# Kernel optimization log

Measured on AMD Instinct MI355X. Metric: run time of the kernel, lower is better.

Reference implementation:

```python
import math
import jax, jax.numpy as jnp
import numpy as np

N_HEAD = 16

def setup_inputs() -> dict:
    key = jax.random.key(0)
    ks = jax.random.split(key, 7)
    B, T, C = 4, 2048, 1024
    QL, KVL = 256, 256
    s = 0.02
    return {
        "x":     jax.random.normal(ks[0], (B, T, C), jnp.float32),
        "W_dq":  jax.random.normal(ks[1], (QL, C), jnp.float32) * s,
        "W_uq":  jax.random.normal(ks[2], (C, QL), jnp.float32) * s,
        "W_dkv": jax.random.normal(ks[3], (KVL, C), jnp.float32) * s,
        "W_uk":  jax.random.normal(ks[4], (C, KVL), jnp.float32) * s,
        "W_uv":  jax.random.normal(ks[5], (C, KVL), jnp.float32) * s,
        "W_o":   jax.random.normal(ks[6], (C, C), jnp.float32) * s,
    }

def reference(x, W_dq, W_uq, W_dkv, W_uk, W_uv, W_o):
    B, T, C = x.shape
    nh = N_HEAD
    hs = C // nh
    kvl = W_dkv.shape[0]
    # Absorbed projection matrices (training path: recomputed each call)
    # k_eff: (nh, hs, kvl); v_eff: (nh, kvl, hs)
    k_eff = (W_dq.T @ W_uq.T @ W_uk).reshape(nh, hs, kvl)
    v_eff = (W_uv.T @ W_o.T).reshape(kvl, nh, hs).transpose(1, 0, 2)
    # Latent KV cache: (B, T, kvl)
    c_kv = x @ W_dkv.T
    # Queries: (B, nh, T, hs)
    q = (x @ W_dq.T @ W_uq.T).reshape(B, T, nh, hs).transpose(0, 2, 1, 3)
    # Scores: q @ k_eff @ c_kv^T / sqrt(hs) -> (B, nh, T, T)
    q_lat = jnp.einsum('bhtd,hdl->bhtl', q, k_eff)
    attn = jnp.einsum('bhtl,bsl->bhts', q_lat, c_kv) / math.sqrt(hs)
    causal_mask = jnp.triu(jnp.ones((T, T), bool), k=1)
    attn = jnp.where(causal_mask[None, None], -jnp.inf, attn)
    attn = jax.nn.softmax(attn, axis=-1)  # dropout p=0 -> identity
    # Output: attn @ c_kv @ v_eff -> (B, T, C)
    ctx = jnp.einsum('bhts,bsl->bhtl', attn, c_kv)
    y = jnp.einsum('bhtl,hld->bhtd', ctx, v_eff).transpose(0, 2, 1, 3).reshape(B, T, C)
    return (y, c_kv)
```

## Files before the change

kernel.cpp:

```cpp
#include <hip/hip_runtime.h>

typedef unsigned short u16;
typedef __attribute__((ext_vector_type(8))) short short8;
typedef __attribute__((ext_vector_type(4))) float f32x4;

#define MFMA_BF16 __builtin_amdgcn_mfma_f32_16x16x32_bf16

__device__ __forceinline__ u16 f2bf(float f){
  unsigned int u = __builtin_bit_cast(unsigned int, f);
  u += 0x7fffu + ((u >> 16) & 1u);
  return (u16)(u >> 16);
}

__device__ __forceinline__ void gld16(const void* g, void* l){
  __builtin_amdgcn_global_load_lds(
      (const __attribute__((address_space(1))) unsigned int*)g,
      (__attribute__((address_space(3))) unsigned int*)l, 16, 0, 0);
}

__global__ void k_transpose4(const float* __restrict__ s0, float* __restrict__ d0,
                             const float* __restrict__ s1, float* __restrict__ d1,
                             const float* __restrict__ s2, float* __restrict__ d2,
                             const float* __restrict__ s3, float* __restrict__ d3)
{
  __shared__ float tile[32][33];
  int z = blockIdx.z;
  const float* src = z == 0 ? s0 : z == 1 ? s1 : z == 2 ? s2 : s3;
  float* dst       = z == 0 ? d0 : z == 1 ? d1 : z == 2 ? d2 : d3;
  int rows = z == 0 ? 256 : 1024, cols = z == 0 ? 1024 : 256;
  int c0 = blockIdx.x * 32, r0 = blockIdx.y * 32;
  if (c0 >= cols || r0 >= rows) return;
  int tx = threadIdx.x, ty = threadIdx.y;
#pragma unroll
  for (int i = 0; i < 4; ++i){
    int r = ty + i * 8;
    tile[r][tx] = src[(long)(r0 + r) * cols + c0 + tx];
  }
  __syncthreads();
#pragma unroll
  for (int i = 0; i < 4; ++i){
    int r = ty + i * 8;
    dst[(long)(c0 + r) * rows + r0 + tx] = tile[tx][r];
  }
}

__global__ __launch_bounds__(256)
void k_gemm_nt(const float* __restrict__ A, const float* __restrict__ B,
               float* __restrict__ Cf, u16* __restrict__ Cb,
               int M, int N, int K, int lda, int ldb, int ldc,
               long sA, long sB, long sC, float scale)
{
  A += (long)blockIdx.z * sA; B += (long)blockIdx.z * sB;
  if (Cf) Cf += (long)blockIdx.z * sC;
  if (Cb) Cb += (long)blockIdx.z * sC;
  const int n0 = blockIdx.x * 64, m0 = blockIdx.y * 64;
  const int tid = threadIdx.x;
  const int wave = tid >> 6, lane = tid & 63, quad = lane >> 4, l16 = lane & 15;
  __shared__ u16 As[64 * 40];
  __shared__ u16 Bs[64 * 40];
  f32x4 acc[4];
#pragma unroll
  for (int n = 0; n < 4; ++n) acc[n] = (f32x4){0.f, 0.f, 0.f, 0.f};

  const int lr = tid >> 2;
  const int lc = (tid & 3) * 8;
  for (int k0 = 0; k0 < K; k0 += 32){
    {
      const float* pa = &A[(long)(m0 + lr) * lda + k0 + lc];
      float4 a0 = *(const float4*)pa;
      float4 a1 = *(const float4*)(pa + 4);
      short8 pk;
      pk[0]=(short)f2bf(a0.x); pk[1]=(short)f2bf(a0.y); pk[2]=(short)f2bf(a0.z); pk[3]=(short)f2bf(a0.w);
      pk[4]=(short)f2bf(a1.x); pk[5]=(short)f2bf(a1.y); pk[6]=(short)f2bf(a1.z); pk[7]=(short)f2bf(a1.w);
      *(short8*)&As[lr * 40 + lc] = pk;
      const float* pb = &B[(long)(n0 + lr) * ldb + k0 + lc];
      float4 b0 = *(const float4*)pb;
      float4 b1 = *(const float4*)(pb + 4);
      short8 qk;
      qk[0]=(short)f2bf(b0.x); qk[1]=(short)f2bf(b0.y); qk[2]=(short)f2bf(b0.z); qk[3]=(short)f2bf(b0.w);
      qk[4]=(short)f2bf(b1.x); qk[5]=(short)f2bf(b1.y); qk[6]=(short)f2bf(b1.z); qk[7]=(short)f2bf(b1.w);
      *(short8*)&Bs[lr * 40 + lc] = qk;
    }
    __syncthreads();
    short8 a = *(const short8*)&As[(wave * 16 + l16) * 40 + quad * 8];
#pragma unroll
    for (int n = 0; n < 4; ++n){
      short8 b = *(const short8*)&Bs[(n * 16 + l16) * 40 + quad * 8];
      acc[n] = MFMA_BF16(a, b, acc[n], 0, 0, 0);
    }
    __syncthreads();
  }
#pragma unroll
  for (int n = 0; n < 4; ++n)
#pragma unroll
    for (int r = 0; r < 4; ++r){
      int row = m0 + wave * 16 + quad * 4 + r;
      int col = n0 + n * 16 + l16;
      float v = acc[n][r] * scale;
      if (Cf) Cf[(long)row * ldc + col] = v;
      if (Cb) Cb[(long)row * ldc + col] = f2bf(v);
    }
}

__global__ __launch_bounds__(256)
void k_proj(const float* __restrict__ x, const float* __restrict__ Wdq,
            const float* __restrict__ Wdkv, u16* __restrict__ xq,
            float* __restrict__ ckv_f, u16* __restrict__ ckv_bf, u16* __restrict__ ckvT)
{
  const bool is_kv = blockIdx.x >= 4;
  const float* B = is_kv ? Wdkv : Wdq;
  const int n0 = (blockIdx.x & 3) * 64, m0 = blockIdx.y * 64;
  const int tid = threadIdx.x;
  const int wave = tid >> 6, lane = tid & 63, quad = lane >> 4, l16 = lane & 15;
  __shared__ u16 As[64 * 40];
  __shared__ u16 Bs[64 * 40];
  f32x4 acc[4];
#pragma unroll
  for (int n = 0; n < 4; ++n) acc[n] = (f32x4){0.f, 0.f, 0.f, 0.f};

  const int lr = tid >> 2;
  const int lc = (tid & 3) * 8;
  for (int k0 = 0; k0 < 1024; k0 += 32){
    {
      const float* pa = &x[(long)(m0 + lr) * 1024 + k0 + lc];
      float4 a0 = *(const float4*)pa;
      float4 a1 = *(const float4*)(pa + 4);
      short8 pk;
      pk[0]=(short)f2bf(a0.x); pk[1]=(short)f2bf(a0.y); pk[2]=(short)f2bf(a0.z); pk[3]=(short)f2bf(a0.w);
      pk[4]=(short)f2bf(a1.x); pk[5]=(short)f2bf(a1.y); pk[6]=(short)f2bf(a1.z); pk[7]=(short)f2bf(a1.w);
      *(short8*)&As[lr * 40 + lc] = pk;
      const float* pb = &B[(long)(n0 + lr) * 1024 + k0 + lc];
      float4 b0 = *(const float4*)pb;
      float4 b1 = *(const float4*)(pb + 4);
      short8 qk;
      qk[0]=(short)f2bf(b0.x); qk[1]=(short)f2bf(b0.y); qk[2]=(short)f2bf(b0.z); qk[3]=(short)f2bf(b0.w);
      qk[4]=(short)f2bf(b1.x); qk[5]=(short)f2bf(b1.y); qk[6]=(short)f2bf(b1.z); qk[7]=(short)f2bf(b1.w);
      *(short8*)&Bs[lr * 40 + lc] = qk;
    }
    __syncthreads();
    short8 a = *(const short8*)&As[(wave * 16 + l16) * 40 + quad * 8];
#pragma unroll
    for (int n = 0; n < 4; ++n){
      short8 b = *(const short8*)&Bs[(n * 16 + l16) * 40 + quad * 8];
      acc[n] = MFMA_BF16(a, b, acc[n], 0, 0, 0);
    }
    __syncthreads();
  }
  if (!is_kv){
#pragma unroll
    for (int n = 0; n < 4; ++n)
#pragma unroll
      for (int r = 0; r < 4; ++r){
        int row = m0 + wave * 16 + quad * 4 + r;
        int col = n0 + n * 16 + l16;
        xq[(long)row * 256 + col] = f2bf(acc[n][r]);
      }
  } else {
    const int b = (m0 >> 11);
    const int t0 = (m0 & 2047) + wave * 16 + quad * 4;
#pragma unroll
    for (int n = 0; n < 4; ++n){
      int col = n0 + n * 16 + l16;
      u16 pk[4];
#pragma unroll
      for (int r = 0; r < 4; ++r){
        int row = m0 + wave * 16 + quad * 4 + r;
        float v = acc[n][r];
        ckv_f [(long)row * 256 + col] = v;
        ckv_bf[(long)row * 256 + col] = f2bf(v);
        pk[r] = f2bf(v);
      }
      *(uint2*)&ckvT[((long)b * 256 + col) * 2048 + t0] = *(uint2*)pk;
    }
  }
}

__global__ __launch_bounds__(256, 2)
void k_flash(const u16* __restrict__ xq, const u16* __restrict__ Pt,
             const u16* __restrict__ ckv_bf, const u16* __restrict__ ckvT,
             const u16* __restrict__ Vt, float* __restrict__ y)
{
  const int qt = 31 - blockIdx.x, h = blockIdx.y, b = blockIdx.z;
  const int tid = threadIdx.x;
  const int wg = tid >> 6, lane = tid & 63, quad = lane >> 4, l16 = lane & 15;

  __shared__ u16 X0[64 * 256];
  __shared__ u16 X1[256 * 64];

  const int trow = wg * 16 + l16;
  const long tglob = (long)b * 2048 + qt * 64;
  const int sw_t = trow & 7;

  const u16* ckv_b  = ckv_bf + (long)b * 2048 * 256;
  const u16* ckvT_b = ckvT   + (long)b * 256 * 2048;

  const u16* srcA[8]; const u16* srcB[8];
  {
    int l5 = lane >> 5, g32 = lane & 31;
#pragma unroll
    for (int j = 0; j < 8; ++j){
      int s = (wg * 8 + j) * 2 + l5;
      int g = g32 ^ (s & 7);
      srcA[j] = ckv_b + (long)s * 256 + g * 8;
    }
    int l3 = lane >> 3, g8 = lane & 7;
#pragma unroll
    for (int j = 0; j < 8; ++j){
      int l = (wg * 8 + j) * 8 + l3;
      int g = g8 ^ (l & 7);
      srcB[j] = ckvT_b + (long)l * 2048 + g * 8;
    }
  }

  short8 aS[8];
  {
    short8 bq[8];
    const u16* xr = xq + (tglob + trow) * 256;
#pragma unroll
    for (int ks = 0; ks < 8; ++ks)
      bq[ks] = *(const short8*)&xr[ks * 32 + quad * 8];
    const u16* pth = Pt + (long)h * 65536;
#pragma unroll
    for (int mb = 0; mb < 16; ++mb){
      f32x4 acc = (f32x4){0.f, 0.f, 0.f, 0.f};
#pragma unroll
      for (int ks = 0; ks < 8; ++ks){
        short8 pa = *(const short8*)&pth[(mb * 16 + l16) * 256 + ks * 32 + quad * 8];
        acc = MFMA_BF16(pa, bq[ks], acc, 0, 0, 0);
      }
#pragma unroll
      for (int r = 0; r < 4; ++r){
        int l = mb * 16 + quad * 4 + r;
        int cs = (((l >> 3) ^ (l16 & 7)) << 3) | (l & 7);
        X0[trow * 256 + cs] = f2bf(acc[r]);
      }
    }
  }
  __syncthreads();
#pragma unroll
  for (int ks = 0; ks < 8; ++ks){
    int gl = ks * 4 + quad;
    aS[ks] = *(const short8*)&X0[trow * 256 + ((gl ^ sw_t) << 3)];
  }

  float m_t = -1e30f, l_t = 0.f;
  f32x4 oacc[16];
#pragma unroll
  for (int n = 0; n < 16; ++n) oacc[n] = (f32x4){0.f, 0.f, 0.f, 0.f};

  for (int st = 0; st <= qt; ++st){
    __syncthreads();
#pragma unroll
    for (int j = 0; j < 8; ++j)
      gld16(srcA[j] + (long)st * 16384, &X0[(wg * 8 + j) * 512]);
#pragma unroll
    for (int j = 0; j < 8; ++j)
      gld16(srcB[j] + st * 64, &X1[(wg * 8 + j) * 512]);
    __syncthreads();

    f32x4 sacc[4];
#pragma unroll
    for (int mb = 0; mb < 4; ++mb) sacc[mb] = (f32x4){0.f, 0.f, 0.f, 0.f};
#pragma unroll
    for (int ks = 0; ks < 8; ++ks){
#pragma unroll
      for (int mb = 0; mb < 4; ++mb){
        int gl = ks * 4 + quad;
        short8 a = *(const short8*)&X0[(mb * 16 + l16) * 256 + ((gl ^ (l16 & 7)) << 3)];
        sacc[mb] = MFMA_BF16(a, aS[ks], sacc[mb], 0, 0, 0);
      }
    }
    if (st == qt){
      int t = qt * 64 + trow;
#pragma unroll
      for (int mb = 0; mb < 4; ++mb)
#pragma unroll
        for (int r = 0; r < 4; ++r)
          if (st * 64 + mb * 16 + quad * 4 + r > t) sacc[mb][r] = -1e30f;
    }

    float pm[4][4];
    {
      float rm = sacc[0][0];
#pragma unroll
      for (int mb = 0; mb < 4; ++mb)
#pragma unroll
        for (int r = 0; r < 4; ++r) rm = fmaxf(rm, sacc[mb][r]);
      rm = fmaxf(rm, __shfl_xor(rm, 16, 64));
      rm = fmaxf(rm, __shfl_xor(rm, 32, 64));
      float mnew = fmaxf(m_t, rm);
      float alpha = __expf(m_t - mnew);
      m_t = mnew;
      float rs = 0.f;
#pragma unroll
      for (int mb = 0; mb < 4; ++mb)
#pragma unroll
        for (int r = 0; r < 4; ++r){
          float pe = __expf(sacc[mb][r] - mnew);
          pm[mb][r] = pe;
          rs += pe;
        }
      rs += __shfl_xor(rs, 16, 64);
      rs += __shfl_xor(rs, 32, 64);
      l_t = l_t * alpha + rs;
#pragma unroll
      for (int r2 = 0; r2 < 4; ++r2){
        float ar = __shfl(alpha, quad * 4 + r2, 64);
#pragma unroll
        for (int n = 0; n < 16; ++n) oacc[n][r2] *= ar;
      }
    }
    __syncthreads();
#pragma unroll
    for (int mb = 0; mb < 4; ++mb)
#pragma unroll
      for (int r = 0; r < 4; ++r)
        X0[trow * 72 + mb * 16 + quad * 4 + r] = f2bf(pm[mb][r]);
    __syncthreads();

    {
      short8 a0 = *(const short8*)&X0[trow * 72 + quad * 8];
      short8 a1 = *(const short8*)&X0[trow * 72 + 32 + quad * 8];
#pragma unroll
      for (int n = 0; n < 16; ++n){
        int lr_ = n * 16 + l16;
        int swl = lr_ & 7;
        short8 b0 = *(const short8*)&X1[lr_ * 64 + ((quad ^ swl) << 3)];
        short8 b1 = *(const short8*)&X1[lr_ * 64 + (((4 + quad) ^ swl) << 3)];
        oacc[n] = MFMA_BF16(a0, b0, oacc[n], 0, 0, 0);
        oacc[n] = MFMA_BF16(a1, b1, oacc[n], 0, 0, 0);
      }
    }
  }

  __syncthreads();
  {
    float linv = 1.f / l_t;
#pragma unroll
    for (int r = 0; r < 4; ++r){
      float lr_ = __shfl(linv, quad * 4 + r, 64);
#pragma unroll
      for (int n = 0; n < 16; ++n) oacc[n][r] *= lr_;
    }
#pragma unroll
    for (int n = 0; n < 16; ++n)
#pragma unroll
      for (int r = 0; r < 4; ++r){
        int trw = wg * 16 + quad * 4 + r;
        int l = n * 16 + l16;
        int cs = (((l >> 3) ^ (trw & 7)) << 3) | (l & 7);
        X0[trw * 256 + cs] = f2bf(oacc[n][r]);
      }
  }
  __syncthreads();
  {
    const u16* vth = Vt + (long)h * 64 * 256;
    short8 ca[8];
#pragma unroll
    for (int ks = 0; ks < 8; ++ks){
      int gl = ks * 4 + quad;
      ca[ks] = *(const short8*)&X0[trow * 256 + ((gl ^ sw_t) << 3)];
    }
#pragma unroll
    for (int n = 0; n < 4; ++n){
      f32x4 acc = (f32x4){0.f, 0.f, 0.f, 0.f};
#pragma unroll
      for (int ks = 0; ks < 8; ++ks){
        short8 vb = *(const short8*)&vth[(n * 16 + l16) * 256 + ks * 32 + quad * 8];
        acc = MFMA_BF16(ca[ks], vb, acc, 0, 0, 0);
      }
#pragma unroll
      for (int r = 0; r < 4; ++r)
        y[(tglob + wg * 16 + quad * 4 + r) * 1024 + h * 64 + n * 16 + l16] = acc[r];
    }
  }
}

extern "C" void kernel_launch(void* const* d_in, const int* in_sizes, int n_in,
                              void* d_out, int out_size, void* d_ws, size_t ws_size,
                              hipStream_t stream)
{
  (void)in_sizes; (void)n_in; (void)out_size; (void)ws_size;
  const float* x    = (const float*)d_in[0];
  const float* Wdq  = (const float*)d_in[1];
  const float* Wuq  = (const float*)d_in[2];
  const float* Wdkv = (const float*)d_in[3];
  const float* Wuk  = (const float*)d_in[4];
  const float* Wuv  = (const float*)d_in[5];
  const float* Wo   = (const float*)d_in[6];

  float* y_out   = (float*)d_out;
  float* ckv_out = y_out + (size_t)4 * 2048 * 1024;

  char* base = (char*)d_ws;
  float* wdqT   = (float*)(base + 0);
  float* wuqT   = (float*)(base + 1048576);
  float* wukT   = (float*)(base + 2097152);
  float* wuvT   = (float*)(base + 3145728);
  u16*   ckvT   = (u16*)  (base + 0);
  float* t1T    = (float*)(base + 4194304);
  float* keffT  = (float*)(base + 4456448);
  u16*   pt     = (u16*)  (base + 5505024);
  u16*   vt     = (u16*)  (base + 7602176);
  u16*   xq     = (u16*)  (base + 8126464);
  u16*   ckv_bf = (u16*)  (base + 12320768);

  k_transpose4<<<dim3(32, 32, 4), dim3(32, 8), 0, stream>>>(
      Wdq, wdqT, Wuq, wuqT, Wuk, wukT, Wuv, wuvT);

  k_gemm_nt<<<dim3(4, 4, 1), 256, 0, stream>>>(wukT, wuqT, t1T, (u16*)0,
      256, 256, 1024, 1024, 1024, 256, 0, 0, 0, 1.f);
  k_gemm_nt<<<dim3(16, 4, 1), 256, 0, stream>>>(t1T, wdqT, keffT, (u16*)0,
      256, 1024, 256, 256, 256, 1024, 0, 0, 0, 1.f);
  k_gemm_nt<<<dim3(4, 4, 16), 256, 0, stream>>>(keffT, wuqT, (float*)0, pt,
      256, 256, 64, 1024, 1024, 256, 64, 64, 65536, 0.125f);
  k_gemm_nt<<<dim3(4, 16, 1), 256, 0, stream>>>(Wo, wuvT, (float*)0, vt,
      1024, 256, 1024, 1024, 1024, 256, 0, 0, 0, 1.f);

  k_proj<<<dim3(8, 128), 256, 0, stream>>>(x, Wdq, Wdkv, xq, ckv_out, ckv_bf, ckvT);

  k_flash<<<dim3(32, 16, 4), 256, 0, stream>>>(xq, pt, ckv_bf, ckvT, vt, y_out);
}
```

Before: 740.0 us.

## Widen flash attention blocks to 128 query rows with 8 waves sharing KV tiles

The flash kernel now runs 512 threads per block covering 128 query rows, so each latent KV tile loaded into LDS is reused by twice as many waves and total KV traffic roughly halves. Waves skip score and PV work on tiles that lie fully above the causal diagonal. The P tile is written per wave into LDS without the extra block barrier, using packed stores and a swizzle. In exchange the block count halves, register pressure rises under the 512,4 launch bound, and waves near the diagonal sit idle while their block-mates finish the extra tiles.

```diff
diff --git a/kernel.cpp b/kernel.cpp
--- a/kernel.cpp
+++ b/kernel.cpp
@@ -175,12 +175,12 @@
   }
 }
 
-__global__ __launch_bounds__(256, 2)
+__global__ __launch_bounds__(512, 4)
 void k_flash(const u16* __restrict__ xq, const u16* __restrict__ Pt,
              const u16* __restrict__ ckv_bf, const u16* __restrict__ ckvT,
              const u16* __restrict__ Vt, float* __restrict__ y)
 {
-  const int qt = 31 - blockIdx.x, h = blockIdx.y, b = blockIdx.z;
+  const int qt = 15 - (int)blockIdx.x, h = blockIdx.y, b = blockIdx.z;
   const int tid = threadIdx.x;
   const int wg = tid >> 6, lane = tid & 63, quad = lane >> 4, l16 = lane & 15;
 
@@ -188,27 +188,25 @@
   __shared__ u16 X1[256 * 64];
 
   const int trow = wg * 16 + l16;
-  const long tglob = (long)b * 2048 + qt * 64;
-  const int sw_t = trow & 7;
+  const long tglob = (long)b * 2048 + (long)qt * 128;
+  u16* Xq = (wg < 4) ? X0 : X1;
+  const int rloc = trow & 63;
+  const int sw7 = l16 & 7;
 
   const u16* ckv_b  = ckv_bf + (long)b * 2048 * 256;
   const u16* ckvT_b = ckvT   + (long)b * 256 * 2048;
 
-  const u16* srcA[8]; const u16* srcB[8];
+  int offA[4], offB[4];
   {
     int l5 = lane >> 5, g32 = lane & 31;
-#pragma unroll
-    for (int j = 0; j < 8; ++j){
-      int s = (wg * 8 + j) * 2 + l5;
-      int g = g32 ^ (s & 7);
-      srcA[j] = ckv_b + (long)s * 256 + g * 8;
-    }
     int l3 = lane >> 3, g8 = lane & 7;
 #pragma unroll
-    for (int j = 0; j < 8; ++j){
-      int l = (wg * 8 + j) * 8 + l3;
-      int g = g8 ^ (l & 7);
-      srcB[j] = ckvT_b + (long)l * 2048 + g * 8;
+    for (int j = 0; j < 4; ++j){
+      int c = wg * 4 + j;
+      int s = c * 2 + l5;
+      offA[j] = s * 256 + ((g32 ^ (s & 7)) * 8);
+      int l = c * 8 + l3;
+      offB[j] = l * 2048 + ((g8 ^ (l & 7)) * 8);
     }
   }
 
@@ -231,16 +229,15 @@
 #pragma unroll
       for (int r = 0; r < 4; ++r){
         int l = mb * 16 + quad * 4 + r;
-        int cs = (((l >> 3) ^ (l16 & 7)) << 3) | (l & 7);
-        X0[trow * 256 + cs] = f2bf(acc[r]);
-      }
-    }
-  }
-  __syncthreads();
+        int cs = (((l >> 3) ^ sw7) << 3) | (l & 7);
+        Xq[rloc * 256 + cs] = f2bf(acc[r]);
+      }
+    }
+  }
 #pragma unroll
   for (int ks = 0; ks < 8; ++ks){
     int gl = ks * 4 + quad;
-    aS[ks] = *(const short8*)&X0[trow * 256 + ((gl ^ sw_t) << 3)];
+    aS[ks] = *(const short8*)&Xq[rloc * 256 + ((gl ^ sw7) << 3)];
   }
 
   float m_t = -1e30f, l_t = 0.f;
@@ -248,39 +245,41 @@
 #pragma unroll
   for (int n = 0; n < 16; ++n) oacc[n] = (f32x4){0.f, 0.f, 0.f, 0.f};
 
-  for (int st = 0; st <= qt; ++st){
-    __syncthreads();
-#pragma unroll
-    for (int j = 0; j < 8; ++j)
-      gld16(srcA[j] + (long)st * 16384, &X0[(wg * 8 + j) * 512]);
-#pragma unroll
-    for (int j = 0; j < 8; ++j)
-      gld16(srcB[j] + st * 64, &X1[(wg * 8 + j) * 512]);
-    __syncthreads();
-
+  const int nst = 2 * qt + 2;
+  const int tmin_w = qt * 128 + wg * 16;
+
+  for (int st = 0; st < nst; ++st){
+    __syncthreads();
+#pragma unroll
+    for (int j = 0; j < 4; ++j)
+      gld16(ckv_b + (long)st * 16384 + offA[j], &X0[(wg * 4 + j) * 512]);
+#pragma unroll
+    for (int j = 0; j < 4; ++j)
+      gld16(ckvT_b + st * 64 + offB[j], &X1[(wg * 4 + j) * 512]);
+    __syncthreads();
+
+    const bool active = (st * 64 <= tmin_w + 15);
     f32x4 sacc[4];
-#pragma unroll
-    for (int mb = 0; mb < 4; ++mb) sacc[mb] = (f32x4){0.f, 0.f, 0.f, 0.f};
-#pragma unroll
-    for (int ks = 0; ks < 8; ++ks){
-#pragma unroll
-      for (int mb = 0; mb < 4; ++mb){
-        int gl = ks * 4 + quad;
-        short8 a = *(const short8*)&X0[(mb * 16 + l16) * 256 + ((gl ^ (l16 & 7)) << 3)];
-        sacc[mb] = MFMA_BF16(a, aS[ks], sacc[mb], 0, 0, 0);
-      }
-    }
-    if (st == qt){
-      int t = qt * 64 + trow;
-#pragma unroll
-      for (int mb = 0; mb < 4; ++mb)
-#pragma unroll
-        for (int r = 0; r < 4; ++r)
-          if (st * 64 + mb * 16 + quad * 4 + r > t) sacc[mb][r] = -1e30f;
-    }
-
-    float pm[4][4];
-    {
+    if (active){
+#pragma unroll
+      for (int mb = 0; mb < 4; ++mb) sacc[mb] = (f32x4){0.f, 0.f, 0.f, 0.f};
+#pragma unroll
+      for (int ks = 0; ks < 8; ++ks){
+#pragma unroll
+        for (int mb = 0; mb < 4; ++mb){
+          int gl = ks * 4 + quad;
+          short8 a = *(const short8*)&X0[(mb * 16 + l16) * 256 + ((gl ^ (l16 & 7)) << 3)];
+          sacc[mb] = MFMA_BF16(a, aS[ks], sacc[mb], 0, 0, 0);
+        }
+      }
+      if ((st + 1) * 64 > tmin_w + 1){
+        int t = qt * 128 + trow;
+#pragma unroll
+        for (int mb = 0; mb < 4; ++mb)
+#pragma unroll
+          for (int r = 0; r < 4; ++r)
+            if (st * 64 + mb * 16 + quad * 4 + r > t) sacc[mb][r] = -1e30f;
+      }
       float rm = sacc[0][0];
 #pragma unroll
       for (int mb = 0; mb < 4; ++mb)
@@ -297,7 +296,7 @@
 #pragma unroll
         for (int r = 0; r < 4; ++r){
           float pe = __expf(sacc[mb][r] - mnew);
-          pm[mb][r] = pe;
+          sacc[mb][r] = pe;
           rs += pe;
         }
       rs += __shfl_xor(rs, 16, 64);
@@ -311,16 +310,19 @@
       }
     }
     __syncthreads();
-#pragma unroll
-    for (int mb = 0; mb < 4; ++mb)
-#pragma unroll
-      for (int r = 0; r < 4; ++r)
-        X0[trow * 72 + mb * 16 + quad * 4 + r] = f2bf(pm[mb][r]);
-    __syncthreads();
-
-    {
-      short8 a0 = *(const short8*)&X0[trow * 72 + quad * 8];
-      short8 a1 = *(const short8*)&X0[trow * 72 + 32 + quad * 8];
+
+    if (active){
+#pragma unroll
+      for (int mb = 0; mb < 4; ++mb){
+        u16 pk[4];
+#pragma unroll
+        for (int r = 0; r < 4; ++r) pk[r] = f2bf(sacc[mb][r]);
+        int c = mb * 16 + quad * 4;
+        int gr = (c >> 3) ^ sw7;
+        *(uint2*)&X0[trow * 64 + gr * 8 + (c & 7)] = *(uint2*)pk;
+      }
+      short8 a0 = *(const short8*)&X0[trow * 64 + ((quad ^ sw7) << 3)];
+      short8 a1 = *(const short8*)&X0[trow * 64 + (((4 + quad) ^ sw7) << 3)];
 #pragma unroll
       for (int n = 0; n < 16; ++n){
         int lr_ = n * 16 + l16;
@@ -349,17 +351,16 @@
         int trw = wg * 16 + quad * 4 + r;
         int l = n * 16 + l16;
         int cs = (((l >> 3) ^ (trw & 7)) << 3) | (l & 7);
-        X0[trw * 256 + cs] = f2bf(oacc[n][r]);
-      }
-  }
-  __syncthreads();
+        Xq[(trw & 63) * 256 + cs] = f2bf(oacc[n][r]);
+      }
+  }
   {
     const u16* vth = Vt + (long)h * 64 * 256;
     short8 ca[8];
 #pragma unroll
     for (int ks = 0; ks < 8; ++ks){
       int gl = ks * 4 + quad;
-      ca[ks] = *(const short8*)&X0[trow * 256 + ((gl ^ sw_t) << 3)];
+      ca[ks] = *(const short8*)&Xq[rloc * 256 + ((gl ^ sw7) << 3)];
     }
 #pragma unroll
     for (int n = 0; n < 4; ++n){
@@ -419,5 +420,5 @@
 
   k_proj<<<dim3(8, 128), 256, 0, stream>>>(x, Wdq, Wdkv, xq, ckv_out, ckv_bf, ckvT);
 
-  k_flash<<<dim3(32, 16, 4), 256, 0, stream>>>(xq, pt, ckv_bf, ckvT, vt, y_out);
-}
+  k_flash<<<dim3(16, 16, 4), 512, 0, stream>>>(xq, pt, ckv_bf, ckvT, vt, y_out);
+}
```

Result: slower. 885.2 us (+19.6%).

## Load K/V tiles directly from global memory and use per-wave LDS slabs

Applied to the files above, without the earlier changes.

The flash kernel no longer stages the ckv and ckvT tiles into shared memory with global_load_lds and block-wide barriers. Each wave now reads its MFMA operands straight from global memory (relying on L1/L2 for reuse across the four waves) and uses a small private padded LDS slab for its own layout transposes, which removes every __syncthreads. The smaller shared-memory footprint lets the launch bounds ask for three blocks per CU. The cost is that each wave fetches the same K/V data separately, and the strided ckvT reads (2048-element row stride) are poorly coalesced, so global and cache traffic rises.

```diff
diff --git a/kernel.cpp b/kernel.cpp
--- a/kernel.cpp
+++ b/kernel.cpp
@@ -10,12 +10,6 @@
   unsigned int u = __builtin_bit_cast(unsigned int, f);
   u += 0x7fffu + ((u >> 16) & 1u);
   return (u16)(u >> 16);
-}
-
-__device__ __forceinline__ void gld16(const void* g, void* l){
-  __builtin_amdgcn_global_load_lds(
-      (const __attribute__((address_space(1))) unsigned int*)g,
-      (__attribute__((address_space(3))) unsigned int*)l, 16, 0, 0);
 }
 
 __global__ void k_transpose4(const float* __restrict__ s0, float* __restrict__ d0,
@@ -175,42 +169,23 @@
   }
 }
 
-__global__ __launch_bounds__(256, 2)
+__global__ __launch_bounds__(256, 3)
 void k_flash(const u16* __restrict__ xq, const u16* __restrict__ Pt,
              const u16* __restrict__ ckv_bf, const u16* __restrict__ ckvT,
              const u16* __restrict__ Vt, float* __restrict__ y)
 {
-  const int qt = 31 - blockIdx.x, h = blockIdx.y, b = blockIdx.z;
+  const int qt = 31 - (int)blockIdx.x, h = blockIdx.y, b = blockIdx.z;
   const int tid = threadIdx.x;
   const int wg = tid >> 6, lane = tid & 63, quad = lane >> 4, l16 = lane & 15;
 
-  __shared__ u16 X0[64 * 256];
-  __shared__ u16 X1[256 * 64];
+  __shared__ u16 slab[4][16 * 264];
+  u16* sw = slab[wg];
 
   const int trow = wg * 16 + l16;
-  const long tglob = (long)b * 2048 + qt * 64;
-  const int sw_t = trow & 7;
+  const long tglob = (long)b * 2048 + (long)qt * 64;
 
   const u16* ckv_b  = ckv_bf + (long)b * 2048 * 256;
   const u16* ckvT_b = ckvT   + (long)b * 256 * 2048;
-
-  const u16* srcA[8]; const u16* srcB[8];
-  {
-    int l5 = lane >> 5, g32 = lane & 31;
-#pragma unroll
-    for (int j = 0; j < 8; ++j){
-      int s = (wg * 8 + j) * 2 + l5;
-      int g = g32 ^ (s & 7);
-      srcA[j] = ckv_b + (long)s * 256 + g * 8;
-    }
-    int l3 = lane >> 3, g8 = lane & 7;
-#pragma unroll
-    for (int j = 0; j < 8; ++j){
-      int l = (wg * 8 + j) * 8 + l3;
-      int g = g8 ^ (l & 7);
-      srcB[j] = ckvT_b + (long)l * 2048 + g * 8;
-    }
-  }
 
   short8 aS[8];
   {
@@ -228,20 +203,15 @@
         short8 pa = *(const short8*)&pth[(mb * 16 + l16) * 256 + ks * 32 + quad * 8];
         acc = MFMA_BF16(pa, bq[ks], acc, 0, 0, 0);
       }
-#pragma unroll
-      for (int r = 0; r < 4; ++r){
-        int l = mb * 16 + quad * 4 + r;
-        int cs = (((l >> 3) ^ (l16 & 7)) << 3) | (l & 7);
-        X0[trow * 256 + cs] = f2bf(acc[r]);
-      }
-    }
-  }
-  __syncthreads();
-#pragma unroll
-  for (int ks = 0; ks < 8; ++ks){
-    int gl = ks * 4 + quad;
-    aS[ks] = *(const short8*)&X0[trow * 256 + ((gl ^ sw_t) << 3)];
-  }
+      u16 pk[4];
+#pragma unroll
+      for (int r = 0; r < 4; ++r) pk[r] = f2bf(acc[r]);
+      *(uint2*)&sw[l16 * 264 + mb * 16 + quad * 4] = *(uint2*)pk;
+    }
+  }
+#pragma unroll
+  for (int ks = 0; ks < 8; ++ks)
+    aS[ks] = *(const short8*)&sw[l16 * 264 + ks * 32 + quad * 8];
 
   float m_t = -1e30f, l_t = 0.f;
   f32x4 oacc[16];
@@ -249,14 +219,8 @@
   for (int n = 0; n < 16; ++n) oacc[n] = (f32x4){0.f, 0.f, 0.f, 0.f};
 
   for (int st = 0; st <= qt; ++st){
-    __syncthreads();
-#pragma unroll
-    for (int j = 0; j < 8; ++j)
-      gld16(srcA[j] + (long)st * 16384, &X0[(wg * 8 + j) * 512]);
-#pragma unroll
-    for (int j = 0; j < 8; ++j)
-      gld16(srcB[j] + st * 64, &X1[(wg * 8 + j) * 512]);
-    __syncthreads();
+    const u16* pA = ckv_b + (long)st * 16384;
+    const u16* pB = ckvT_b + st * 64;
 
     f32x4 sacc[4];
 #pragma unroll
@@ -265,8 +229,7 @@
     for (int ks = 0; ks < 8; ++ks){
 #pragma unroll
       for (int mb = 0; mb < 4; ++mb){
-        int gl = ks * 4 + quad;
-        short8 a = *(const short8*)&X0[(mb * 16 + l16) * 256 + ((gl ^ (l16 & 7)) << 3)];
+        short8 a = *(const short8*)&pA[(mb * 16 + l16) * 256 + ks * 32 + quad * 8];
         sacc[mb] = MFMA_BF16(a, aS[ks], sacc[mb], 0, 0, 0);
       }
     }
@@ -279,7 +242,6 @@
           if (st * 64 + mb * 16 + quad * 4 + r > t) sacc[mb][r] = -1e30f;
     }
 
-    float pm[4][4];
     {
       float rm = sacc[0][0];
 #pragma unroll
@@ -297,7 +259,7 @@
 #pragma unroll
         for (int r = 0; r < 4; ++r){
           float pe = __expf(sacc[mb][r] - mnew);
-          pm[mb][r] = pe;
+          sacc[mb][r] = pe;
           rs += pe;
         }
       rs += __shfl_xor(rs, 16, 64);
@@ -310,30 +272,27 @@
         for (int n = 0; n < 16; ++n) oacc[n][r2] *= ar;
       }
     }
-    __syncthreads();
-#pragma unroll
-    for (int mb = 0; mb < 4; ++mb)
-#pragma unroll
-      for (int r = 0; r < 4; ++r)
-        X0[trow * 72 + mb * 16 + quad * 4 + r] = f2bf(pm[mb][r]);
-    __syncthreads();
-
-    {
-      short8 a0 = *(const short8*)&X0[trow * 72 + quad * 8];
-      short8 a1 = *(const short8*)&X0[trow * 72 + 32 + quad * 8];
-#pragma unroll
-      for (int n = 0; n < 16; ++n){
-        int lr_ = n * 16 + l16;
-        int swl = lr_ & 7;
-        short8 b0 = *(const short8*)&X1[lr_ * 64 + ((quad ^ swl) << 3)];
-        short8 b1 = *(const short8*)&X1[lr_ * 64 + (((4 + quad) ^ swl) << 3)];
-        oacc[n] = MFMA_BF16(a0, b0, oacc[n], 0, 0, 0);
-        oacc[n] = MFMA_BF16(a1, b1, oacc[n], 0, 0, 0);
-      }
-    }
-  }
-
-  __syncthreads();
+
+#pragma unroll
+    for (int mb = 0; mb < 4; ++mb){
+      u16 pk[4];
+#pragma unroll
+      for (int r = 0; r < 4; ++r) pk[r] = f2bf(sacc[mb][r]);
+      *(uint2*)&sw[l16 * 72 + mb * 16 + quad * 4] = *(uint2*)pk;
+    }
+    short8 a0 = *(const short8*)&sw[l16 * 72 + quad * 8];
+    short8 a1 = *(const short8*)&sw[l16 * 72 + 32 + quad * 8];
+
+#pragma unroll
+    for (int n = 0; n < 16; ++n){
+      const u16* pr = &pB[(n * 16 + l16) * 2048 + quad * 8];
+      short8 b0 = *(const short8*)pr;
+      short8 b1 = *(const short8*)(pr + 32);
+      oacc[n] = MFMA_BF16(a0, b0, oacc[n], 0, 0, 0);
+      oacc[n] = MFMA_BF16(a1, b1, oacc[n], 0, 0, 0);
+    }
+  }
+
   {
     float linv = 1.f / l_t;
 #pragma unroll
@@ -345,22 +304,15 @@
 #pragma unroll
     for (int n = 0; n < 16; ++n)
 #pragma unroll
-      for (int r = 0; r < 4; ++r){
-        int trw = wg * 16 + quad * 4 + r;
-        int l = n * 16 + l16;
-        int cs = (((l >> 3) ^ (trw & 7)) << 3) | (l & 7);
-        X0[trw * 256 + cs] = f2bf(oacc[n][r]);
-      }
-  }
-  __syncthreads();
+      for (int r = 0; r < 4; ++r)
+        sw[(quad * 4 + r) * 264 + n * 16 + l16] = f2bf(oacc[n][r]);
+  }
   {
     const u16* vth = Vt + (long)h * 64 * 256;
     short8 ca[8];
 #pragma unroll
-    for (int ks = 0; ks < 8; ++ks){
-      int gl = ks * 4 + quad;
-      ca[ks] = *(const short8*)&X0[trow * 256 + ((gl ^ sw_t) << 3)];
-    }
+    for (int ks = 0; ks < 8; ++ks)
+      ca[ks] = *(const short8*)&sw[l16 * 264 + ks * 32 + quad * 8];
 #pragma unroll
     for (int n = 0; n < 4; ++n){
       f32x4 acc = (f32x4){0.f, 0.f, 0.f, 0.f};
```

Result: slower. 2.369 ms (+220.1%).
